# Optimization experiments

Hardware: AMD Instinct MI355X
Metric: run time of the kernel (lower is better)

Reference implementation:

```python
import jax, jax.numpy as jnp
import numpy as np

TEMPERATURE = 0.1
POS_WINDOW = 1
NEG_WINDOW = 10


def setup_inputs() -> dict:
    key = jax.random.key(0)
    img_feats = jax.random.normal(key, (8, 2048, 256), dtype=jnp.float32)
    return {"img_feats": img_feats}


def reference(img_feats):
    B, S, D = img_feats.shape
    # L2-normalize along feature dim (matches F.normalize(dim=-1))
    x = img_feats / jnp.clip(jnp.linalg.norm(img_feats, axis=-1, keepdims=True), 1e-12)
    # Full pairwise cosine similarity, scaled by temperature: [B, S, S]
    sim = jnp.einsum('bsd,btd->bst', x, x) / TEMPERATURE

    idx = jnp.arange(S)
    diff = jnp.abs(idx[:, None] - idx[None, :])  # |anchor - other|, [S, S]
    pos_mask = (diff >= 1) & (diff <= POS_WINDOW)   # temporal positives
    neg_mask = diff >= NEG_WINDOW                   # temporal negatives

    # Anchors are valid only if they have >=1 positive and >=1 negative
    pos_count = jnp.sum(pos_mask, axis=1)  # [S]
    valid_t = (pos_count > 0) & (jnp.sum(neg_mask, axis=1) > 0)  # [S]

    E = jnp.exp(sim)  # plain exp, matching the original (no max-subtraction)
    # Per-anchor sum of exp over negatives: [B, S]
    neg_sum = jnp.einsum('bst,st->bs', E, neg_mask.astype(sim.dtype))

    # Per positive pair: -log(exp(sp) / (exp(sp) + neg_sum)) = log(exp(sp)+neg_sum) - sp
    per_pair = jnp.log(E + neg_sum[:, :, None]) - sim  # [B, S, S]
    w = (pos_mask & valid_t[:, None]).astype(sim.dtype)  # [S, S]
    total_loss = jnp.einsum('bst,st->', per_pair, w)

    n_valid = B * jnp.sum(jnp.where(valid_t, pos_count, 0))
    return jnp.where(n_valid > 0, total_loss / n_valid.astype(sim.dtype), 0.0)
```

## Files before the change

kernel.cpp:

```cpp
#include <hip/hip_runtime.h>

#define BATCH 8
#define SEQ   2048
#define DIM   256
#define TINV  10.0f
#define NEGW  10

#define BM 128
#define BN 128
#define BK 64
#define NTILE (SEQ / BM)
#define NPAIR (NTILE * (NTILE + 1) / 2)

typedef float f32x4  __attribute__((ext_vector_type(4)));
typedef short bf16x8 __attribute__((ext_vector_type(8)));

__device__ __forceinline__ unsigned short f2b(float f) {
  union { float f; unsigned u; } v; v.f = f;
  unsigned r = v.u + 0x7fffu + ((v.u >> 16) & 1u);
  return (unsigned short)(r >> 16);
}
__device__ __forceinline__ float b2f(unsigned short u) {
  union { unsigned u; float f; } v; v.u = ((unsigned)u) << 16;
  return v.f;
}

__global__ void normalize_bf16_kernel(const float* __restrict__ x,
                                      unsigned short* __restrict__ xb,
                                      float* __restrict__ zero_region) {
  if (blockIdx.x < 64) {
    zero_region[blockIdx.x * 256 + threadIdx.x] = 0.f;
  } else if (blockIdx.x == 64 && threadIdx.x < 16) {
    zero_region[16384 + threadIdx.x] = 0.f;
  }
  int row  = blockIdx.x * 4 + (threadIdx.x >> 6);
  int lane = threadIdx.x & 63;
  const float4 v = reinterpret_cast<const float4*>(x + (size_t)row * DIM)[lane];
  float ss = v.x * v.x + v.y * v.y + v.z * v.z + v.w * v.w;
#pragma unroll
  for (int off = 32; off; off >>= 1) ss += __shfl_xor(ss, off, 64);
  float rn = 1.0f / fmaxf(sqrtf(ss), 1e-12f);
  ushort4 o;
  o.x = f2b(v.x * rn); o.y = f2b(v.y * rn);
  o.z = f2b(v.z * rn); o.w = f2b(v.w * rn);
  reinterpret_cast<ushort4*>(xb + (size_t)row * DIM)[lane] = o;
}

__device__ __forceinline__ void stage8(const unsigned short* __restrict__ G,
                                       unsigned short* dst_wave_uniform,
                                       int rowbase, int rl, int p, int kt) {
  int row = rowbase + rl;
  const unsigned short* src =
      G + (size_t)row * DIM + kt * BK + ((p ^ (row & 7)) << 3);
  __builtin_amdgcn_global_load_lds(
      (const __attribute__((address_space(1))) void*)src,
      (__attribute__((address_space(3))) void*)dst_wave_uniform, 16, 0, 0);
}

__global__ __launch_bounds__(256, 1)
void sim_negsum_kernel(const unsigned short* __restrict__ xb,
                       float* __restrict__ negsum,
                       float* __restrict__ sp_out) {
  const int b = blockIdx.y;
  int ti = 0, rem = blockIdx.x;
  while (rem >= NTILE - ti) { rem -= NTILE - ti; ti++; }
  const int tj = ti + rem;
  const bool diag = (ti == tj);
  const int s0 = ti * BM, t0 = tj * BN;

  __shared__ unsigned short Asm4[4][BM * BK];
  __shared__ unsigned short Bsm4[4][BM * BK];

  const unsigned short* Ag = xb + (size_t)b * SEQ * DIM + (size_t)s0 * DIM;
  const unsigned short* Bg = diag ? Ag
      : xb + (size_t)b * SEQ * DIM + (size_t)t0 * DIM;

  const int tid  = threadIdx.x;
  const int wid  = tid >> 6;
  const int lane = tid & 63;
  const int wm   = wid >> 1;
  const int wn   = wid & 1;
  const int kg   = lane >> 4;
  const int cl   = lane & 15;
  const int rl   = lane >> 3;
  const int p    = lane & 7;

  f32x4 acc[4][4];
#pragma unroll
  for (int m = 0; m < 4; ++m)
#pragma unroll
    for (int n = 0; n < 4; ++n)
      acc[m][n] = (f32x4){0.f, 0.f, 0.f, 0.f};

#pragma unroll
  for (int kt = 0; kt < 4; ++kt) {
#pragma unroll
    for (int it = 0; it < 4; ++it) {
      int rowbase = wid * 32 + it * 8;
      stage8(Ag, &Asm4[kt][rowbase * BK], rowbase, rl, p, kt);
      stage8(Bg, &Bsm4[kt][rowbase * BK], rowbase, rl, p, kt);
    }
  }

#define CONSUME(KT)                                                           \
  do {                                                                        \
    const char* Acur = (const char*)&Asm4[KT][0];                             \
    const char* Bcur = (const char*)&Bsm4[KT][0];                             \
    _Pragma("unroll")                                                         \
    for (int kk = 0; kk < BK / 32; ++kk) {                                    \
      bf16x8 af[4], bfr[4];                                                   \
      _Pragma("unroll")                                                       \
      for (int m = 0; m < 4; ++m) {                                           \
        int r = wm * 64 + m * 16 + cl;                                        \
        int slot = kk * 4 + kg;                                               \
        af[m] = *reinterpret_cast<const bf16x8*>(                             \
            Acur + r * 128 + ((slot ^ (r & 7)) << 4));                        \
      }                                                                       \
      _Pragma("unroll")                                                       \
      for (int n = 0; n < 4; ++n) {                                           \
        int r = wn * 64 + n * 16 + cl;                                        \
        int slot = kk * 4 + kg;                                               \
        bfr[n] = *reinterpret_cast<const bf16x8*>(                            \
            Bcur + r * 128 + ((slot ^ (r & 7)) << 4));                        \
      }                                                                       \
      _Pragma("unroll")                                                       \
      for (int m = 0; m < 4; ++m)                                             \
        _Pragma("unroll")                                                     \
        for (int n = 0; n < 4; ++n)                                           \
          acc[m][n] = __builtin_amdgcn_mfma_f32_16x16x32_bf16(                \
              af[m], bfr[n], acc[m][n], 0, 0, 0);                             \
    }                                                                         \
  } while (0)

#define SYNC_VM(VM)                                                           \
  asm volatile("s_waitcnt vmcnt(" #VM ")" ::: "memory");                      \
  __builtin_amdgcn_s_barrier();                                               \
  asm volatile("" ::: "memory");

  SYNC_VM(24) CONSUME(0);
  SYNC_VM(16) CONSUME(1);
  SYNC_VM(8)  CONSUME(2);
  SYNC_VM(0)  CONSUME(3);
#undef CONSUME
#undef SYNC_VM

  float rowpart[4][4];
  float colpart[4];
#pragma unroll
  for (int m = 0; m < 4; ++m)
#pragma unroll
    for (int r = 0; r < 4; ++r) rowpart[m][r] = 0.f;
#pragma unroll
  for (int n = 0; n < 4; ++n) colpart[n] = 0.f;

#pragma unroll
  for (int m = 0; m < 4; ++m) {
#pragma unroll
    for (int n = 0; n < 4; ++n) {
#pragma unroll
      for (int r = 0; r < 4; ++r) {
        int srow = s0 + wm * 64 + m * 16 + (kg << 2) + r;
        int tcol = t0 + wn * 64 + n * 16 + cl;
        int diff = tcol - srow;
        int d = diff < 0 ? -diff : diff;
        float e = (d >= NEGW) ? __expf(acc[m][n][r] * TINV) : 0.f;
        rowpart[m][r] += e;
        colpart[n]    += e;
        if (diff == 1)
          sp_out[(size_t)b * (SEQ - 1) + srow] = acc[m][n][r] * TINV;
      }
    }
  }

#pragma unroll
  for (int off = 1; off <= 8; off <<= 1)
#pragma unroll
    for (int m = 0; m < 4; ++m)
#pragma unroll
      for (int r = 0; r < 4; ++r)
        rowpart[m][r] += __shfl_xor(rowpart[m][r], off, 64);
  if (cl == 0) {
#pragma unroll
    for (int m = 0; m < 4; ++m)
#pragma unroll
      for (int r = 0; r < 4; ++r)
        atomicAdd(&negsum[(size_t)b * SEQ + s0 + wm * 64 + m * 16 + (kg << 2) + r],
                  rowpart[m][r]);
  }

  if (!diag) {
#pragma unroll
    for (int off = 16; off <= 32; off <<= 1)
#pragma unroll
      for (int n = 0; n < 4; ++n)
        colpart[n] += __shfl_xor(colpart[n], off, 64);
    if (lane < 16) {
#pragma unroll
      for (int n = 0; n < 4; ++n)
        atomicAdd(&negsum[(size_t)b * SEQ + t0 + wn * 64 + n * 16 + lane],
                  colpart[n]);
    }
  }
}

__device__ __forceinline__ int negcnt(int s) {
  int a = s - (NEGW - 1);      if (a < 0) a = 0;
  int b = SEQ - NEGW - s;      if (b < 0) b = 0;
  return a + b;
}

#define POSFIN_BLOCKS 64

__global__ __launch_bounds__(256)
void pos_fin_kernel(const float* __restrict__ sp,
                    const float* __restrict__ negsum,
                    float* __restrict__ loss,
                    unsigned int* __restrict__ ticket,
                    float* __restrict__ out) {
  __shared__ float red[4];
  __shared__ int   nvr[4];
  const int NP = BATCH * (SEQ - 1);
  int pidx = blockIdx.x * 256 + threadIdx.x;
  float term = 0.f;
  if (pidx < NP) {
    int b = pidx / (SEQ - 1), s = pidx % (SEQ - 1);
    float spv = sp[pidx];
    float e = __expf(spv);
    if (negcnt(s) > 0)     term += logf(e + negsum[(size_t)b * SEQ + s])     - spv;
    if (negcnt(s + 1) > 0) term += logf(e + negsum[(size_t)b * SEQ + s + 1]) - spv;
  }
  int cnt = 0;
#pragma unroll
  for (int s = threadIdx.x; s < SEQ; s += 256)
    if (negcnt(s) > 0) cnt += (s > 0) + (s < SEQ - 1);

#pragma unroll
  for (int off = 32; off; off >>= 1) {
    term += __shfl_xor(term, off, 64);
    cnt  += __shfl_xor(cnt,  off, 64);
  }
  if ((threadIdx.x & 63) == 0) {
    red[threadIdx.x >> 6] = term;
    nvr[threadIdx.x >> 6] = cnt;
  }
  __syncthreads();
  if (threadIdx.x == 0) {
    atomicAdd(loss, red[0] + red[1] + red[2] + red[3]);
    long long nv = (long long)BATCH * (nvr[0] + nvr[1] + nvr[2] + nvr[3]);
    __threadfence();
    unsigned int old = atomicAdd(ticket, 1u);
    if (old == POSFIN_BLOCKS - 1) {
      float total = atomicAdd(loss, 0.0f);
      out[0] = (nv > 0) ? total / (float)nv : 0.0f;
    }
  }
}

extern "C" void kernel_launch(void* const* d_in, const int* in_sizes, int n_in,
                              void* d_out, int out_size, void* d_ws, size_t ws_size,
                              hipStream_t stream) {
  const float* x = (const float*)d_in[0];
  unsigned short* xb = (unsigned short*)d_ws;
  const size_t XB_BYTES = (size_t)BATCH * SEQ * DIM * 2;
  const size_t NS_BYTES = (size_t)BATCH * SEQ * 4;
  float* negsum        = (float*)((char*)d_ws + XB_BYTES);
  float* loss          = (float*)((char*)d_ws + XB_BYTES + NS_BYTES);
  unsigned int* ticket = (unsigned int*)((char*)d_ws + XB_BYTES + NS_BYTES + 4);
  float* sp            = (float*)((char*)d_ws + XB_BYTES + NS_BYTES + 64);

  normalize_bf16_kernel<<<(BATCH * SEQ) / 4, 256, 0, stream>>>(x, xb, negsum);

  dim3 g2(NPAIR, BATCH);
  sim_negsum_kernel<<<g2, 256, 0, stream>>>(xb, negsum, sp);

  pos_fin_kernel<<<POSFIN_BLOCKS, 256, 0, stream>>>(sp, negsum, loss, ticket,
                                                    (float*)d_out);
}
```

Baseline: 58.50 us.

## Load MFMA operands directly from global memory instead of staging through LDS

Removes the LDS staging buffers and the global_load_lds pipeline, and has each wave load its bf16 operand fragments straight from global memory (L2/L1) into registers for the MFMA loop. Launch bounds are raised so up to three blocks can share a CU once the 128 KB of LDS per block is gone, aiming to overlap latency through occupancy rather than explicit staging. The cost is redundant global/L1 traffic, since waves sharing a row or column tile each fetch the same data, and no explicit prefetch overlaps loads with MFMA.

```diff
diff --git a/kernel.cpp b/kernel.cpp
--- a/kernel.cpp
+++ b/kernel.cpp
@@ -8,7 +8,6 @@
 
 #define BM 128
 #define BN 128
-#define BK 64
 #define NTILE (SEQ / BM)
 #define NPAIR (NTILE * (NTILE + 1) / 2)
 
@@ -46,18 +45,7 @@
   reinterpret_cast<ushort4*>(xb + (size_t)row * DIM)[lane] = o;
 }
 
-__device__ __forceinline__ void stage8(const unsigned short* __restrict__ G,
-                                       unsigned short* dst_wave_uniform,
-                                       int rowbase, int rl, int p, int kt) {
-  int row = rowbase + rl;
-  const unsigned short* src =
-      G + (size_t)row * DIM + kt * BK + ((p ^ (row & 7)) << 3);
-  __builtin_amdgcn_global_load_lds(
-      (const __attribute__((address_space(1))) void*)src,
-      (__attribute__((address_space(3))) void*)dst_wave_uniform, 16, 0, 0);
-}
-
-__global__ __launch_bounds__(256, 1)
+__global__ __launch_bounds__(256, 3)
 void sim_negsum_kernel(const unsigned short* __restrict__ xb,
                        float* __restrict__ negsum,
                        float* __restrict__ sp_out) {
@@ -68,13 +56,6 @@
   const bool diag = (ti == tj);
   const int s0 = ti * BM, t0 = tj * BN;
 
-  __shared__ unsigned short Asm4[4][BM * BK];
-  __shared__ unsigned short Bsm4[4][BM * BK];
-
-  const unsigned short* Ag = xb + (size_t)b * SEQ * DIM + (size_t)s0 * DIM;
-  const unsigned short* Bg = diag ? Ag
-      : xb + (size_t)b * SEQ * DIM + (size_t)t0 * DIM;
-
   const int tid  = threadIdx.x;
   const int wid  = tid >> 6;
   const int lane = tid & 63;
@@ -82,8 +63,11 @@
   const int wn   = wid & 1;
   const int kg   = lane >> 4;
   const int cl   = lane & 15;
-  const int rl   = lane >> 3;
-  const int p    = lane & 7;
+
+  const unsigned short* Abase =
+      xb + (size_t)b * SEQ * DIM + (size_t)(s0 + wm * 64 + cl) * DIM;
+  const unsigned short* Bbase =
+      xb + (size_t)b * SEQ * DIM + (size_t)(t0 + wn * 64 + cl) * DIM;
 
   f32x4 acc[4][4];
 #pragma unroll
@@ -93,56 +77,22 @@
       acc[m][n] = (f32x4){0.f, 0.f, 0.f, 0.f};
 
 #pragma unroll
-  for (int kt = 0; kt < 4; ++kt) {
-#pragma unroll
-    for (int it = 0; it < 4; ++it) {
-      int rowbase = wid * 32 + it * 8;
-      stage8(Ag, &Asm4[kt][rowbase * BK], rowbase, rl, p, kt);
-      stage8(Bg, &Bsm4[kt][rowbase * BK], rowbase, rl, p, kt);
-    }
-  }
-
-#define CONSUME(KT)                                                           \
-  do {                                                                        \
-    const char* Acur = (const char*)&Asm4[KT][0];                             \
-    const char* Bcur = (const char*)&Bsm4[KT][0];                             \
-    _Pragma("unroll")                                                         \
-    for (int kk = 0; kk < BK / 32; ++kk) {                                    \
-      bf16x8 af[4], bfr[4];                                                   \
-      _Pragma("unroll")                                                       \
-      for (int m = 0; m < 4; ++m) {                                           \
-        int r = wm * 64 + m * 16 + cl;                                        \
-        int slot = kk * 4 + kg;                                               \
-        af[m] = *reinterpret_cast<const bf16x8*>(                             \
-            Acur + r * 128 + ((slot ^ (r & 7)) << 4));                        \
-      }                                                                       \
-      _Pragma("unroll")                                                       \
-      for (int n = 0; n < 4; ++n) {                                           \
-        int r = wn * 64 + n * 16 + cl;                                        \
-        int slot = kk * 4 + kg;                                               \
-        bfr[n] = *reinterpret_cast<const bf16x8*>(                            \
-            Bcur + r * 128 + ((slot ^ (r & 7)) << 4));                        \
-      }                                                                       \
-      _Pragma("unroll")                                                       \
-      for (int m = 0; m < 4; ++m)                                             \
-        _Pragma("unroll")                                                     \
-        for (int n = 0; n < 4; ++n)                                           \
-          acc[m][n] = __builtin_amdgcn_mfma_f32_16x16x32_bf16(                \
-              af[m], bfr[n], acc[m][n], 0, 0, 0);                             \
-    }                                                                         \
-  } while (0)
-
-#define SYNC_VM(VM)                                                           \
-  asm volatile("s_waitcnt vmcnt(" #VM ")" ::: "memory");                      \
-  __builtin_amdgcn_s_barrier();                                               \
-  asm volatile("" ::: "memory");
-
-  SYNC_VM(24) CONSUME(0);
-  SYNC_VM(16) CONSUME(1);
-  SYNC_VM(8)  CONSUME(2);
-  SYNC_VM(0)  CONSUME(3);
-#undef CONSUME
-#undef SYNC_VM
+  for (int kc = 0; kc < DIM / 32; ++kc) {
+    bf16x8 af[4], bfr[4];
+    const int koff = kc * 32 + kg * 8;
+#pragma unroll
+    for (int m = 0; m < 4; ++m)
+      af[m] = *reinterpret_cast<const bf16x8*>(Abase + (size_t)m * 16 * DIM + koff);
+#pragma unroll
+    for (int n = 0; n < 4; ++n)
+      bfr[n] = *reinterpret_cast<const bf16x8*>(Bbase + (size_t)n * 16 * DIM + koff);
+#pragma unroll
+    for (int m = 0; m < 4; ++m)
+#pragma unroll
+      for (int n = 0; n < 4; ++n)
+        acc[m][n] = __builtin_amdgcn_mfma_f32_16x16x32_bf16(
+            af[m], bfr[n], acc[m][n], 0, 0, 0);
+  }
 
   float rowpart[4][4];
   float colpart[4];
```

After: 65.00 us. 1.11x slower.
